# Kernel tuning notes

Hardware: AMD Instinct MI355X
Metric: run time of the kernel (lower is better)

## Reference

```python
import jax, jax.numpy as jnp
from jax import lax
import numpy as np

B, S, D_IN = 2048, 512, 5
H, E_DIM, N_EMB, C_CONV = 64, 32, 64, 32
COMMIT = 0.01


def _lstm_params(key, in_dim, hid):
    ks = jax.random.split(key, 4)
    sc = 1.0 / np.sqrt(hid)
    wih = jax.random.uniform(ks[0], (4 * hid, in_dim), minval=-sc, maxval=sc)
    whh = jax.random.uniform(ks[1], (4 * hid, hid), minval=-sc, maxval=sc)
    bih = jax.random.uniform(ks[2], (4 * hid,), minval=-sc, maxval=sc)
    bhh = jax.random.uniform(ks[3], (4 * hid,), minval=-sc, maxval=sc)
    return wih, whh, bih, bhh


def setup_inputs() -> dict:
    key = jax.random.key(0)
    ks = jax.random.split(key, 12)
    inp = {}
    inp['x'] = jax.random.normal(ks[0], (B, S, D_IN), dtype=jnp.float32)
    inp['conv_w'] = jax.random.normal(ks[1], (C_CONV, D_IN, 3)) * 0.2  # OIH
    inp['conv_b'] = jax.random.normal(ks[2], (C_CONV,)) * 0.05
    inp['bn_g'] = jnp.ones((C_CONV,)) + jax.random.normal(ks[3], (C_CONV,)) * 0.05
    inp['bn_b'] = jax.random.normal(ks[4], (C_CONV,)) * 0.05
    inp['bn_m'] = jax.random.normal(ks[5], (C_CONV,)) * 0.1
    inp['bn_v'] = jax.random.uniform(ks[6], (C_CONV,), minval=0.5, maxval=1.5)
    cw = _lstm_params(ks[7], C_CONV, H)
    cw1 = _lstm_params(jax.random.fold_in(ks[7], 1), H, H)
    vw = _lstm_params(ks[8], D_IN, H)
    vw1 = _lstm_params(jax.random.fold_in(ks[8], 1), H, H)
    for pre, p in (('cnn0', cw), ('cnn1', cw1), ('vq0', vw), ('vq1', vw1)):
        inp[pre + '_wih'], inp[pre + '_whh'], inp[pre + '_bih'], inp[pre + '_bhh'] = p
    inp['proj_w'] = jax.random.normal(ks[9], (E_DIM, H)) * (1.0 / np.sqrt(H))
    inp['proj_b'] = jax.random.normal(ks[10], (E_DIM,)) * 0.05
    xav = np.sqrt(6.0 / (N_EMB + E_DIM))
    inp['codebook'] = jax.random.uniform(ks[11], (N_EMB, E_DIM), minval=-xav, maxval=xav)
    return inp


def _lstm_layer(xs, wih, whh, bih, bhh):
    # xs: [S, B, in] -> (ys [S,B,H], h_final [B,H])
    b = xs.shape[1]
    h0 = jnp.zeros((b, H), xs.dtype)
    bias = bih + bhh

    def step(carry, x_t):
        h, c = carry
        gates = x_t @ wih.T + h @ whh.T + bias
        i, f, g, o = jnp.split(gates, 4, axis=-1)
        c = jax.nn.sigmoid(f) * c + jax.nn.sigmoid(i) * jnp.tanh(g)
        h = jax.nn.sigmoid(o) * jnp.tanh(c)
        return (h, c), h

    (h, c), ys = lax.scan(step, (h0, h0), xs)
    return ys, h


def _forward(x, conv_w, conv_b, bn_g, bn_b, bn_m, bn_v,
             cnn0_wih, cnn0_whh, cnn0_bih, cnn0_bhh,
             cnn1_wih, cnn1_whh, cnn1_bih, cnn1_bhh,
             vq0_wih, vq0_whh, vq0_bih, vq0_bhh,
             vq1_wih, vq1_whh, vq1_bih, vq1_bhh,
             proj_w, proj_b, codebook):
    # CNN stream: conv1d(k=3, pad=1) + BN (eval) + ReLU; dropout = identity (eval)
    x_ncw = jnp.transpose(x, (0, 2, 1))  # [B, D_IN, S]
    y = lax.conv_general_dilated(x_ncw, conv_w, (1,), [(1, 1)],
                                 dimension_numbers=('NCH', 'OIH', 'NCH'))
    y = y + conv_b[None, :, None]
    y = (y - bn_m[None, :, None]) * (bn_g / jnp.sqrt(bn_v + 1e-5))[None, :, None] + bn_b[None, :, None]
    y = jax.nn.relu(y)
    y = jnp.transpose(y, (2, 0, 1))  # [S, B, 32] time-major
    ys, _ = _lstm_layer(y, cnn0_wih, cnn0_whh, cnn0_bih, cnn0_bhh)
    _, cnn_features = _lstm_layer(ys, cnn1_wih, cnn1_whh, cnn1_bih, cnn1_bhh)  # [B, H]

    # VQ stream
    xt = jnp.transpose(x, (1, 0, 2))  # [S, B, D_IN]
    ys2, _ = _lstm_layer(xt, vq0_wih, vq0_whh, vq0_bih, vq0_bhh)
    _, vq_hidden = _lstm_layer(ys2, vq1_wih, vq1_whh, vq1_bih, vq1_bhh)  # [B, H]
    vq_proj = vq_hidden @ proj_w.T + proj_b  # [B, E_DIM]

    # Vector quantization
    d = (jnp.sum(vq_proj ** 2, axis=1, keepdims=True)
         + jnp.sum(codebook ** 2, axis=1)
         - 2.0 * vq_proj @ codebook.T)  # [B, N_EMB]
    idx = jnp.argmin(d, axis=1)
    quantized = codebook[idx]  # [B, E_DIM]
    e_loss = jnp.mean((lax.stop_gradient(quantized) - vq_proj) ** 2)
    q_loss = jnp.mean((quantized - lax.stop_gradient(vq_proj)) ** 2)
    vq_loss = q_loss + COMMIT * e_loss
    quantized = vq_proj + lax.stop_gradient(quantized - vq_proj)  # STE
    enc = jax.nn.one_hot(idx, N_EMB, dtype=vq_proj.dtype)
    avg_probs = jnp.mean(enc, axis=0)
    perplexity = jnp.exp(-jnp.sum(avg_probs * jnp.log(avg_probs + 1e-10)))

    combined = jnp.concatenate([cnn_features, quantized], axis=1)  # [B, H+E_DIM]
    return combined, vq_loss, perplexity


def reference(x, conv_w, conv_b, bn_g, bn_b, bn_m, bn_v,
              cnn0_wih, cnn0_whh, cnn0_bih, cnn0_bhh,
              cnn1_wih, cnn1_whh, cnn1_bih, cnn1_bhh,
              vq0_wih, vq0_whh, vq0_bih, vq0_bhh,
              vq1_wih, vq1_whh, vq1_bih, vq1_bhh,
              proj_w, proj_b, codebook):
    combined, vq_loss, perplexity = _forward(
        x, conv_w, conv_b, bn_g, bn_b, bn_m, bn_v,
        cnn0_wih, cnn0_whh, cnn0_bih, cnn0_bhh,
        cnn1_wih, cnn1_whh, cnn1_bih, cnn1_bhh,
        vq0_wih, vq0_whh, vq0_bih, vq0_bhh,
        vq1_wih, vq1_whh, vq1_bih, vq1_bhh,
        proj_w, proj_b, codebook)
    # num_classes=None -> returns (combined, combined, vq_loss, perplexity)
    return combined, combined, vq_loss, perplexity
```

## Files before the change

### kernel.cpp

```cpp
#include <hip/hip_runtime.h>
#include <math.h>
#include <stdint.h>

#define B_TOT 2048
#define SEQ   512
#define DIN   5
#define HID   64
#define EDIM  32
#define NEMB  64
#define BT    16
#define NBLK_STREAM 128
#define COMB  96
#define OUTC  (B_TOT*COMB)

typedef __attribute__((ext_vector_type(8))) _Float16 half8;
typedef __attribute__((ext_vector_type(4))) float float4v;

#if __has_builtin(__builtin_amdgcn_exp2f)
#define FEXP2(x) __builtin_amdgcn_exp2f(x)
#else
#define FEXP2(x) exp2f(x)
#endif
#if __has_builtin(__builtin_amdgcn_rcpf)
#define FRCP(x) __builtin_amdgcn_rcpf(x)
#else
#define FRCP(x) (1.0f/(x))
#endif

__device__ __forceinline__ float fsig(float x){
  return FRCP(1.0f + FEXP2(-1.44269504089f * x));
}
__device__ __forceinline__ float ftanh(float x){
  return fmaf(2.0f, FRCP(1.0f + FEXP2(-2.88539008178f * x)), -1.0f);
}
#define MFMA16(a,b,c) __builtin_amdgcn_mfma_f32_16x16x32_f16((a),(b),(c),0,0,0)

#define LOOP_BARRIER() do { \
    asm volatile("s_waitcnt lgkmcnt(0)" ::: "memory"); \
    __builtin_amdgcn_s_barrier(); \
  } while (0)

__global__ __launch_bounds__(256)
void conv_pre_kernel(const float* __restrict__ xg,
                     const float* __restrict__ conv_w, const float* __restrict__ conv_b,
                     const float* __restrict__ bn_g, const float* __restrict__ bn_b,
                     const float* __restrict__ bn_m, const float* __restrict__ bn_v,
                     _Float16* __restrict__ Y)
{
  __shared__ float wcs[16][32];
  const int tid = threadIdx.x;
  if (tid < 32) {
    float s = bn_g[tid] * rsqrtf(bn_v[tid] + 1e-5f);
#pragma unroll
    for (int i = 0; i < 5; ++i)
#pragma unroll
      for (int tau = 0; tau < 3; ++tau)
        wcs[tau*5 + i][tid] = conv_w[tid*15 + i*3 + tau] * s;
    wcs[15][tid] = (conv_b[tid] - bn_m[tid]) * s + bn_b[tid];
  }
  __syncthreads();
  const int total = B_TOT * SEQ;
  for (int idx = blockIdx.x*256 + tid; idx < total; idx += gridDim.x*256) {
    const int b = idx >> 9, t = idx & (SEQ-1);
    const float* xb = xg + ((size_t)b*SEQ + t)*DIN;
    float xm[5], x0[5], xp[5];
#pragma unroll
    for (int i = 0; i < 5; ++i) {
      x0[i] = xb[i];
      xm[i] = (t > 0)       ? xb[i - DIN] : 0.f;
      xp[i] = (t < SEQ-1)   ? xb[i + DIN] : 0.f;
    }
    _Float16 yv[32];
#pragma unroll
    for (int ch = 0; ch < 32; ++ch) {
      float s = wcs[15][ch];
#pragma unroll
      for (int i = 0; i < 5; ++i)
        s += wcs[i][ch]*xm[i] + wcs[5+i][ch]*x0[i] + wcs[10+i][ch]*xp[i];
      yv[ch] = (_Float16)fmaxf(s, 0.f);
    }
    half8* dst = (half8*)(Y + (size_t)idx*32);
#pragma unroll
    for (int g = 0; g < 4; ++g) dst[g] = *(half8*)&yv[g*8];
  }
}

template<bool PRE>
__global__ __launch_bounds__(1024)
__attribute__((amdgpu_waves_per_eu(4, 4)))
void fused_kernel(const float* __restrict__ xg,
                  const float* __restrict__ conv_w, const float* __restrict__ conv_b,
                  const float* __restrict__ bn_g, const float* __restrict__ bn_b,
                  const float* __restrict__ bn_m, const float* __restrict__ bn_v,
                  const float* __restrict__ cnn0_wih, const float* __restrict__ cnn0_whh,
                  const float* __restrict__ cnn0_bih, const float* __restrict__ cnn0_bhh,
                  const float* __restrict__ cnn1_wih, const float* __restrict__ cnn1_whh,
                  const float* __restrict__ cnn1_bih, const float* __restrict__ cnn1_bhh,
                  const float* __restrict__ vq0_wih, const float* __restrict__ vq0_whh,
                  const float* __restrict__ vq0_bih, const float* __restrict__ vq0_bhh,
                  const float* __restrict__ vq1_wih, const float* __restrict__ vq1_whh,
                  const float* __restrict__ vq1_bih, const float* __restrict__ vq1_bhh,
                  const float* __restrict__ proj_w, const float* __restrict__ proj_b,
                  const float* __restrict__ codebook, const _Float16* __restrict__ Yg,
                  float* __restrict__ out, float* __restrict__ ws_f,
                  int* __restrict__ ws_hist)
{
  __shared__ __align__(16) _Float16 ZT[2][5][4][BT][8];
  __shared__ __align__(16) float hfin[BT][HID];
  __shared__ __align__(16) float pbuf[BT][EDIM];
  __shared__ float xwin[4][BT][DIN];

  const int tid  = threadIdx.x;
  const bool is_cnn = (blockIdx.x < NBLK_STREAM);
  const int b0   = (is_cnn ? blockIdx.x : blockIdx.x - NBLK_STREAM) * BT;
  const int w    = tid >> 6;
  const int lane = tid & 63;
  const int n16  = lane & 15;
  const int quad = lane >> 4;
  const int u    = 4*w + quad;

  const float* wih0 = is_cnn ? cnn0_wih : vq0_wih;
  const float* whh0 = is_cnn ? cnn0_whh : vq0_whh;
  const float* bih0 = is_cnn ? cnn0_bih : vq0_bih;
  const float* bhh0 = is_cnn ? cnn0_bhh : vq0_bhh;
  const float* wih1 = is_cnn ? cnn1_wih : vq1_wih;
  const float* whh1 = is_cnn ? cnn1_whh : vq1_whh;
  const float* bih1 = is_cnn ? cnn1_bih : vq1_bih;
  const float* bhh1 = is_cnn ? cnn1_bhh : vq1_bhh;

  const int orow = 64*(n16 & 3) + 4*w + (n16 >> 2);
  half8 Ah0[3], Ah1[4];
#pragma unroll
  for (int kt = 0; kt < 3; ++kt) {
    half8 vh;
#pragma unroll
    for (int j = 0; j < 8; ++j) {
      const int g = kt*32 + quad*8 + j;
      float wv;
      if (is_cnn) wv = (g < 32) ? wih0[orow*32 + g] : whh0[orow*64 + (g-32)];
      else        wv = (g < 5) ? wih0[orow*5 + g] : (g < 32 ? 0.f : whh0[orow*64 + (g-32)]);
      vh[j] = (_Float16)wv;
    }
    Ah0[kt] = vh;
  }
#pragma unroll
  for (int kt = 0; kt < 4; ++kt) {
    half8 vh;
#pragma unroll
    for (int j = 0; j < 8; ++j) {
      const int g = kt*32 + quad*8 + j;
      float wv = (g < 64) ? wih1[orow*64 + g] : whh1[orow*64 + (g-64)];
      vh[j] = (_Float16)wv;
    }
    Ah1[kt] = vh;
  }

  float4v bc0, bc1;
#pragma unroll
  for (int r = 0; r < 4; ++r) {
    bc0[r] = bih0[64*r + u] + bhh0[64*r + u];
    bc1[r] = bih1[64*r + u] + bhh1[64*r + u];
  }

  float wr[16];
  if (!PRE) {
#pragma unroll
    for (int i = 0; i < 16; ++i) wr[i] = 0.f;
    if (is_cnn && tid < 512) {
      const int cc = tid >> 4;
      float s = bn_g[cc] * rsqrtf(bn_v[cc] + 1e-5f);
#pragma unroll
      for (int i = 0; i < 5; ++i)
#pragma unroll
        for (int tau = 0; tau < 3; ++tau)
          wr[tau*5 + i] = conv_w[cc*15 + i*3 + tau] * s;
      wr[15] = (conv_b[cc] - bn_m[cc]) * s + bn_b[cc];
    }
  }

  for (int i2 = tid; i2 < 2*5*4*BT*8/2; i2 += 1024) ((uint32_t*)ZT)[i2] = 0;

  const int xn = tid / 5, xi = tid % 5;
  const int yn = tid >> 2, ykg = tid & 3;
  float xpref = 0.f;
  half8 ypref{};
  const _Float16* Yb = nullptr;
  if (PRE && is_cnn && tid < 64)
    Yb = Yg + ((size_t)(b0 + yn)*SEQ)*32 + ykg*8;

  #define ZB(b) ((_Float16*)(&ZT[(b)][0][0][0][0]))
  #define ZIDX(tile,k32,n) (((tile)*4 + (((k32)>>3)&3))*(BT*8) + (n)*8 + ((k32)&7))

  if (!PRE && is_cnn) {
    if (tid < BT*DIN) {
#pragma unroll
      for (int j = 0; j < 4; ++j)
        xwin[j][xn][xi] = xg[((size_t)(b0+xn)*SEQ + j)*DIN + xi];
    }
  }
  __syncthreads();

  if (is_cnn) {
    if (PRE) {
      if (tid < 64) {
        half8 y0 = *(const half8*)(Yb + (size_t)0*32);
        half8 y1 = *(const half8*)(Yb + (size_t)1*32);
        ypref    = *(const half8*)(Yb + (size_t)2*32);
        *(half8*)&ZB(1)[ykg*(BT*8) + yn*8] = y0;
        *(half8*)&ZB(0)[ykg*(BT*8) + yn*8] = y1;
      }
    } else {
      if (tid < 512) {
        const int cc = tid >> 4, cn = tid & 15;
        float s = wr[15];
#pragma unroll
        for (int i = 0; i < 5; ++i)
          s += wr[5+i]*xwin[0][cn][i] + wr[10+i]*xwin[1][cn][i];
        s = fmaxf(s, 0.f);
        ZB(1)[ZIDX(0, cc, cn)] = (_Float16)s;
      }
    }
  } else {
    if (tid < BT*DIN) {
      float x0v = xg[((size_t)(b0+xn)*SEQ + 0)*DIN + xi];
      float x1v = xg[((size_t)(b0+xn)*SEQ + 1)*DIN + xi];
      ZB(1)[ZIDX(0, xi, xn)] = (_Float16)x0v;
      ZB(0)[ZIDX(0, xi, xn)] = (_Float16)x1v;
      xpref = xg[((size_t)(b0+xn)*SEQ + 2)*DIN + xi];
    }
  }
  __syncthreads();

  float c0 = 0.f, c1 = 0.f, h1v = 0.f;
  {
    half8 bt0 = *(const half8*)&ZT[1][0][quad][n16][0];
    half8 bt1 = *(const half8*)&ZT[1][1][quad][n16][0];
    half8 bt2 = *(const half8*)&ZT[1][2][quad][n16][0];
    float4v a0 = bc0;
    a0 = MFMA16(Ah0[0], bt0, a0);
    a0 = MFMA16(Ah0[1], bt1, a0);
    a0 = MFMA16(Ah0[2], bt2, a0);
    c0 = fsig(a0[1])*c0 + fsig(a0[0])*ftanh(a0[2]);
    float h0 = fsig(a0[3])*ftanh(c0);
    ZB(0)[ZIDX(1 + (u>>5), u & 31, n16)] = (_Float16)h0;
  }
  if (!PRE && is_cnn) {
    if (tid < 512) {
      const int cc = tid >> 4, cn = tid & 15;
      float s = wr[15];
#pragma unroll
      for (int i = 0; i < 5; ++i)
        s += wr[i]*xwin[0][cn][i] + wr[5+i]*xwin[1][cn][i]
           + wr[10+i]*xwin[2][cn][i];
      s = fmaxf(s, 0.f);
      ZB(0)[ZIDX(0, cc, cn)] = (_Float16)s;
    }
    if (tid < BT*DIN) xpref = xg[((size_t)(b0+xn)*SEQ + 4)*DIN + xi];
  }
  __syncthreads();

#pragma unroll 2
  for (int t = 0; t < SEQ; ++t) {
    const int rb = t & 1, wrb = rb ^ 1;
    half8 bt0 = *(const half8*)&ZT[rb][0][quad][n16][0];
    half8 bt1 = *(const half8*)&ZT[rb][1][quad][n16][0];
    half8 bt2 = *(const half8*)&ZT[rb][2][quad][n16][0];
    half8 bt3 = *(const half8*)&ZT[rb][3][quad][n16][0];
    half8 bt4 = *(const half8*)&ZT[rb][4][quad][n16][0];
    float4v a1 = bc1, a0 = bc0;
    a1 = MFMA16(Ah1[0], bt1, a1);
    a1 = MFMA16(Ah1[1], bt2, a1);
    a1 = MFMA16(Ah1[2], bt3, a1);
    a1 = MFMA16(Ah1[3], bt4, a1);
    a0 = MFMA16(Ah0[0], bt0, a0);
    a0 = MFMA16(Ah0[1], bt1, a0);
    a0 = MFMA16(Ah0[2], bt2, a0);

    {
      c1 = fsig(a1[1])*c1 + fsig(a1[0])*ftanh(a1[2]);
      float h1 = fsig(a1[3])*ftanh(c1);
      ZB(wrb)[ZIDX(3 + (u>>5), u & 31, n16)] = (_Float16)h1;
      if (is_cnn) h1v = h1;
      else if (t == SEQ-1) hfin[n16][u] = h1;
    }
    {
      c0 = fsig(a0[1])*c0 + fsig(a0[0])*ftanh(a0[2]);
      float h0 = fsig(a0[3])*ftanh(c0);
      ZB(wrb)[ZIDX(1 + (u>>5), u & 31, n16)] = (_Float16)h0;
    }
    if (is_cnn) {
      if (PRE) {
        if (tid < 64) {
          *(half8*)&ZB(wrb)[ykg*(BT*8) + yn*8] = ypref;
          const int tq = t + 3;
          if (tq < SEQ) ypref = *(const half8*)(Yb + (size_t)tq*32);
        }
      } else {
        if (tid < 512) {
          const int cc = tid >> 4, cn = tid & 15;
          const int s1 = (t+1)&3, s2 = (t+2)&3, s3 = (t+3)&3;
          float s = wr[15];
#pragma unroll
          for (int i = 0; i < 5; ++i)
            s += wr[i]*xwin[s1][cn][i] + wr[5+i]*xwin[s2][cn][i]
               + wr[10+i]*xwin[s3][cn][i];
          s = fmaxf(s, 0.f);
          ZB(wrb)[ZIDX(0, cc, cn)] = (_Float16)s;
        }
        if (tid < BT*DIN) {
          xwin[t & 3][xn][xi] = xpref;
          const int tq = t + 5;
          xpref = (tq < SEQ) ? xg[((size_t)(b0+xn)*SEQ + tq)*DIN + xi] : 0.f;
        }
      }
    } else {
      if (tid < BT*DIN) {
        ZB(wrb)[ZIDX(0, xi, xn)] = (_Float16)xpref;
        const int tq = t + 3;
        xpref = (tq < SEQ) ? xg[((size_t)(b0+xn)*SEQ + tq)*DIN + xi] : 0.f;
      }
    }
    LOOP_BARRIER();
  }

  if (is_cnn) {
    const size_t gb = (size_t)(b0 + n16);
    out[gb*COMB + u]        = h1v;
    out[OUTC + gb*COMB + u] = h1v;
  } else {
    if (tid < 512) {
      const int pn = tid >> 5, pe = tid & 31;
      float s = proj_b[pe];
      const float* pw = proj_w + pe*HID;
#pragma unroll
      for (int k = 0; k < HID; ++k) s += hfin[pn][k] * pw[k];
      pbuf[pn][pe] = s;
    }
    __syncthreads();
    {
      const int bb = w;
      const int nn = lane;
      const float* cbn = codebook + nn*EDIM;
      float d = 0.f;
#pragma unroll
      for (int k = 0; k < EDIM; ++k) { float df = pbuf[bb][k] - cbn[k]; d += df*df; }
      int bi = nn;
#pragma unroll
      for (int off = 32; off > 0; off >>= 1) {
        float od = __shfl_down(d, off, 64);
        int   oi = __shfl_down(bi, off, 64);
        if (od < d || (od == d && oi < bi)) { d = od; bi = oi; }
      }
      bi = __shfl(bi, 0, 64);
      float lv = 0.f;
      if (nn < EDIM) {
        float q = codebook[bi*EDIM + nn];
        const size_t gb = (size_t)(b0 + bb);
        out[gb*COMB + HID + nn]        = q;
        out[OUTC + gb*COMB + HID + nn] = q;
        float df = q - pbuf[bb][nn];
        lv = df*df;
      }
#pragma unroll
      for (int off = 32; off > 0; off >>= 1) lv += __shfl_down(lv, off, 64);
      if (nn == 0) { atomicAdd(ws_f, lv); atomicAdd(&ws_hist[bi], 1); }
    }
  }
}

__global__ void zero_ws_kernel(float* ws_f, int* ws_hist) {
  const int t = threadIdx.x;
  if (t == 0) ws_f[0] = 0.f;
  if (t < NEMB) ws_hist[t] = 0;
}

__global__ void vq_finalize_kernel(const float* __restrict__ ws_f,
                                   const int* __restrict__ ws_hist,
                                   float* __restrict__ out) {
  const int t = threadIdx.x;
  float p = (float)ws_hist[t] * (1.0f / (float)B_TOT);
  float e = -p * logf(p + 1e-10f);
#pragma unroll
  for (int off = 32; off > 0; off >>= 1) e += __shfl_down(e, off, 64);
  if (t == 0) {
    float mse = ws_f[0] * (1.0f / (float)(B_TOT * EDIM));
    out[2*OUTC + 0] = mse * 1.01f;
    out[2*OUTC + 1] = expf(e);
  }
}

extern "C" void kernel_launch(void* const* d_in, const int* in_sizes, int n_in,
                              void* d_out, int out_size, void* d_ws, size_t ws_size,
                              hipStream_t stream) {
  const float* x        = (const float*)d_in[0];
  const float* conv_w   = (const float*)d_in[1];
  const float* conv_b   = (const float*)d_in[2];
  const float* bn_g     = (const float*)d_in[3];
  const float* bn_b     = (const float*)d_in[4];
  const float* bn_m     = (const float*)d_in[5];
  const float* bn_v     = (const float*)d_in[6];
  const float* cnn0_wih = (const float*)d_in[7];
  const float* cnn0_whh = (const float*)d_in[8];
  const float* cnn0_bih = (const float*)d_in[9];
  const float* cnn0_bhh = (const float*)d_in[10];
  const float* cnn1_wih = (const float*)d_in[11];
  const float* cnn1_whh = (const float*)d_in[12];
  const float* cnn1_bih = (const float*)d_in[13];
  const float* cnn1_bhh = (const float*)d_in[14];
  const float* vq0_wih  = (const float*)d_in[15];
  const float* vq0_whh  = (const float*)d_in[16];
  const float* vq0_bih  = (const float*)d_in[17];
  const float* vq0_bhh  = (const float*)d_in[18];
  const float* vq1_wih  = (const float*)d_in[19];
  const float* vq1_whh  = (const float*)d_in[20];
  const float* vq1_bih  = (const float*)d_in[21];
  const float* vq1_bhh  = (const float*)d_in[22];
  const float* proj_w   = (const float*)d_in[23];
  const float* proj_b   = (const float*)d_in[24];
  const float* codebook = (const float*)d_in[25];

  float* out     = (float*)d_out;
  float* ws_f    = (float*)d_ws;
  int*   ws_hist = (int*)d_ws + 16;

  const size_t Y_BYTES = (size_t)B_TOT * SEQ * 32 * sizeof(_Float16);
  _Float16* Yg = (_Float16*)((char*)d_ws + 1024);
  const bool use_pre = (ws_size >= 1024 + Y_BYTES);

  hipLaunchKernelGGL(zero_ws_kernel, dim3(1), dim3(64), 0, stream, ws_f, ws_hist);
  if (use_pre) {
    hipLaunchKernelGGL(conv_pre_kernel, dim3(1024), dim3(256), 0, stream,
                       x, conv_w, conv_b, bn_g, bn_b, bn_m, bn_v, Yg);
    hipLaunchKernelGGL((fused_kernel<true>), dim3(2*NBLK_STREAM), dim3(1024), 0, stream,
                       x, conv_w, conv_b, bn_g, bn_b, bn_m, bn_v,
                       cnn0_wih, cnn0_whh, cnn0_bih, cnn0_bhh,
                       cnn1_wih, cnn1_whh, cnn1_bih, cnn1_bhh,
                       vq0_wih, vq0_whh, vq0_bih, vq0_bhh,
                       vq1_wih, vq1_whh, vq1_bih, vq1_bhh,
                       proj_w, proj_b, codebook, Yg, out, ws_f, ws_hist);
  } else {
    hipLaunchKernelGGL((fused_kernel<false>), dim3(2*NBLK_STREAM), dim3(1024), 0, stream,
                       x, conv_w, conv_b, bn_g, bn_b, bn_m, bn_v,
                       cnn0_wih, cnn0_whh, cnn0_bih, cnn0_bhh,
                       cnn1_wih, cnn1_whh, cnn1_bih, cnn1_bhh,
                       vq0_wih, vq0_whh, vq0_bih, vq0_bhh,
                       vq1_wih, vq1_whh, vq1_bih, vq1_bhh,
                       proj_w, proj_b, codebook, Yg, out, ws_f, ws_hist);
  }
  hipLaunchKernelGGL(vq_finalize_kernel, dim3(1), dim3(64), 0, stream, ws_f, ws_hist, out);
}
```

Before: 609.5 us.

## Fold bias into activations, split MFMA chains, fuse zero/finalize kernels, retile conv

```diff
diff --git a/kernel.cpp b/kernel.cpp
--- a/kernel.cpp
+++ b/kernel.cpp
@@ -14,6 +14,7 @@
 #define OUTC  (B_TOT*COMB)
 
 typedef __attribute__((ext_vector_type(8))) _Float16 half8;
+typedef __attribute__((ext_vector_type(4))) _Float16 half4;
 typedef __attribute__((ext_vector_type(4))) float float4v;
 
 #if __has_builtin(__builtin_amdgcn_exp2f)
@@ -27,11 +28,20 @@
 #define FRCP(x) (1.0f/(x))
 #endif
 
+#define L2E  1.44269504089f
+#define L2E2 2.88539008178f
+
+__device__ __forceinline__ float sig_b(float a, float bp){
+  return FRCP(1.0f + FEXP2(fmaf(a, -L2E, bp)));
+}
+__device__ __forceinline__ float tanh_b(float a, float bp){
+  return fmaf(2.0f, FRCP(1.0f + FEXP2(fmaf(a, -L2E2, bp))), -1.0f);
+}
+__device__ __forceinline__ float ftanh(float x){
+  return fmaf(2.0f, FRCP(1.0f + FEXP2(-L2E2 * x)), -1.0f);
+}
 __device__ __forceinline__ float fsig(float x){
-  return FRCP(1.0f + FEXP2(-1.44269504089f * x));
-}
-__device__ __forceinline__ float ftanh(float x){
-  return fmaf(2.0f, FRCP(1.0f + FEXP2(-2.88539008178f * x)), -1.0f);
+  return FRCP(1.0f + FEXP2(-L2E * x));
 }
 #define MFMA16(a,b,c) __builtin_amdgcn_mfma_f32_16x16x32_f16((a),(b),(c),0,0,0)
 
@@ -45,43 +55,52 @@
                      const float* __restrict__ conv_w, const float* __restrict__ conv_b,
                      const float* __restrict__ bn_g, const float* __restrict__ bn_b,
                      const float* __restrict__ bn_m, const float* __restrict__ bn_v,
-                     _Float16* __restrict__ Y)
+                     _Float16* __restrict__ Y,
+                     float* __restrict__ ws_f, int* __restrict__ ws_hist,
+                     int* __restrict__ ws_cnt)
 {
-  __shared__ float wcs[16][32];
   const int tid = threadIdx.x;
-  if (tid < 32) {
-    float s = bn_g[tid] * rsqrtf(bn_v[tid] + 1e-5f);
+  if (blockIdx.x == 0) {
+    if (tid == 0) ws_f[0] = 0.f;
+    if (tid < NEMB) ws_hist[tid] = 0;
+    if (tid == 64) ws_cnt[0] = 0;
+  }
+  const int cg = tid & 7;
+  const int it = tid >> 3;
+  float wv[4][15], bz[4];
+#pragma unroll
+  for (int j = 0; j < 4; ++j) {
+    const int ch = cg*4 + j;
+    const float s = bn_g[ch] * rsqrtf(bn_v[ch] + 1e-5f);
 #pragma unroll
     for (int i = 0; i < 5; ++i)
 #pragma unroll
       for (int tau = 0; tau < 3; ++tau)
-        wcs[tau*5 + i][tid] = conv_w[tid*15 + i*3 + tau] * s;
-    wcs[15][tid] = (conv_b[tid] - bn_m[tid]) * s + bn_b[tid];
-  }
-  __syncthreads();
-  const int total = B_TOT * SEQ;
-  for (int idx = blockIdx.x*256 + tid; idx < total; idx += gridDim.x*256) {
-    const int b = idx >> 9, t = idx & (SEQ-1);
-    const float* xb = xg + ((size_t)b*SEQ + t)*DIN;
+        wv[j][tau*5 + i] = conv_w[ch*15 + i*3 + tau] * s;
+    bz[j] = (conv_b[ch] - bn_m[ch]) * s + bn_b[ch];
+  }
+  const int ngrp = (B_TOT * SEQ) / 32;
+  for (int grp = blockIdx.x; grp < ngrp; grp += gridDim.x) {
+    const int idx = grp*32 + it;
+    const int t = idx & (SEQ-1);
+    const float* xb = xg + (size_t)idx*DIN;
     float xm[5], x0[5], xp[5];
 #pragma unroll
     for (int i = 0; i < 5; ++i) {
       x0[i] = xb[i];
-      xm[i] = (t > 0)       ? xb[i - DIN] : 0.f;
-      xp[i] = (t < SEQ-1)   ? xb[i + DIN] : 0.f;
-    }
-    _Float16 yv[32];
-#pragma unroll
-    for (int ch = 0; ch < 32; ++ch) {
-      float s = wcs[15][ch];
+      xm[i] = (t > 0)     ? xb[i - DIN] : 0.f;
+      xp[i] = (t < SEQ-1) ? xb[i + DIN] : 0.f;
+    }
+    half4 yv;
+#pragma unroll
+    for (int j = 0; j < 4; ++j) {
+      float s = bz[j];
 #pragma unroll
       for (int i = 0; i < 5; ++i)
-        s += wcs[i][ch]*xm[i] + wcs[5+i][ch]*x0[i] + wcs[10+i][ch]*xp[i];
-      yv[ch] = (_Float16)fmaxf(s, 0.f);
-    }
-    half8* dst = (half8*)(Y + (size_t)idx*32);
-#pragma unroll
-    for (int g = 0; g < 4; ++g) dst[g] = *(half8*)&yv[g*8];
+        s += wv[j][i]*xm[i] + wv[j][5+i]*x0[i] + wv[j][10+i]*xp[i];
+      yv[j] = (_Float16)fmaxf(s, 0.f);
+    }
+    *(half4*)(Y + (size_t)idx*32 + cg*4) = yv;
   }
 }
 
@@ -103,7 +122,7 @@
                   const float* __restrict__ proj_w, const float* __restrict__ proj_b,
                   const float* __restrict__ codebook, const _Float16* __restrict__ Yg,
                   float* __restrict__ out, float* __restrict__ ws_f,
-                  int* __restrict__ ws_hist)
+                  int* __restrict__ ws_hist, int* __restrict__ ws_cnt)
 {
   __shared__ __align__(16) _Float16 ZT[2][5][4][BT][8];
   __shared__ __align__(16) float hfin[BT][HID];
@@ -155,12 +174,14 @@
     Ah1[kt] = vh;
   }
 
-  float4v bc0, bc1;
+  float bp0[4], bp1[4];
 #pragma unroll
   for (int r = 0; r < 4; ++r) {
-    bc0[r] = bih0[64*r + u] + bhh0[64*r + u];
-    bc1[r] = bih1[64*r + u] + bhh1[64*r + u];
-  }
+    const float k = (r == 2) ? L2E2 : L2E;
+    bp0[r] = -k * (bih0[64*r + u] + bhh0[64*r + u]);
+    bp1[r] = -k * (bih1[64*r + u] + bhh1[64*r + u]);
+  }
+  const float4v zero4 = {0.f, 0.f, 0.f, 0.f};
 
   float wr[16];
   if (!PRE) {
@@ -236,12 +257,14 @@
     half8 bt0 = *(const half8*)&ZT[1][0][quad][n16][0];
     half8 bt1 = *(const half8*)&ZT[1][1][quad][n16][0];
     half8 bt2 = *(const half8*)&ZT[1][2][quad][n16][0];
-    float4v a0 = bc0;
-    a0 = MFMA16(Ah0[0], bt0, a0);
+    float4v a0 = MFMA16(Ah0[0], bt0, zero4);
     a0 = MFMA16(Ah0[1], bt1, a0);
     a0 = MFMA16(Ah0[2], bt2, a0);
-    c0 = fsig(a0[1])*c0 + fsig(a0[0])*ftanh(a0[2]);
-    float h0 = fsig(a0[3])*ftanh(c0);
+    float i0 = sig_b(a0[0], bp0[0]);
+    float g0 = tanh_b(a0[2], bp0[2]);
+    float o0 = sig_b(a0[3], bp0[3]);
+    c0 = i0 * g0;
+    float h0 = o0 * ftanh(c0);
     ZB(0)[ZIDX(1 + (u>>5), u & 31, n16)] = (_Float16)h0;
   }
   if (!PRE && is_cnn) {
@@ -267,25 +290,35 @@
     half8 bt2 = *(const half8*)&ZT[rb][2][quad][n16][0];
     half8 bt3 = *(const half8*)&ZT[rb][3][quad][n16][0];
     half8 bt4 = *(const half8*)&ZT[rb][4][quad][n16][0];
-    float4v a1 = bc1, a0 = bc0;
-    a1 = MFMA16(Ah1[0], bt1, a1);
-    a1 = MFMA16(Ah1[1], bt2, a1);
-    a1 = MFMA16(Ah1[2], bt3, a1);
-    a1 = MFMA16(Ah1[3], bt4, a1);
-    a0 = MFMA16(Ah0[0], bt0, a0);
-    a0 = MFMA16(Ah0[1], bt1, a0);
-    a0 = MFMA16(Ah0[2], bt2, a0);
-
+    float4v p1 = MFMA16(Ah1[0], bt1, zero4);
+    float4v q1 = MFMA16(Ah1[1], bt2, zero4);
+    float4v p0 = MFMA16(Ah0[0], bt0, zero4);
+    p1 = MFMA16(Ah1[2], bt3, p1);
+    q1 = MFMA16(Ah1[3], bt4, q1);
+    p0 = MFMA16(Ah0[1], bt1, p0);
+    p0 = MFMA16(Ah0[2], bt2, p0);
+
+    __builtin_amdgcn_s_setprio(1);
     {
-      c1 = fsig(a1[1])*c1 + fsig(a1[0])*ftanh(a1[2]);
-      float h1 = fsig(a1[3])*ftanh(c1);
+      float a1i = p1[0] + q1[0], a1f = p1[1] + q1[1];
+      float a1g = p1[2] + q1[2], a1o = p1[3] + q1[3];
+      float i1 = sig_b(a1i, bp1[0]);
+      float f1 = sig_b(a1f, bp1[1]);
+      float g1 = tanh_b(a1g, bp1[2]);
+      float o1 = sig_b(a1o, bp1[3]);
+      c1 = fmaf(f1, c1, i1 * g1);
+      float h1 = o1 * ftanh(c1);
       ZB(wrb)[ZIDX(3 + (u>>5), u & 31, n16)] = (_Float16)h1;
       if (is_cnn) h1v = h1;
       else if (t == SEQ-1) hfin[n16][u] = h1;
     }
     {
-      c0 = fsig(a0[1])*c0 + fsig(a0[0])*ftanh(a0[2]);
-      float h0 = fsig(a0[3])*ftanh(c0);
+      float i0 = sig_b(p0[0], bp0[0]);
+      float f0 = sig_b(p0[1], bp0[1]);
+      float g0 = tanh_b(p0[2], bp0[2]);
+      float o0 = sig_b(p0[3], bp0[3]);
+      c0 = fmaf(f0, c0, i0 * g0);
+      float h0 = o0 * ftanh(c0);
       ZB(wrb)[ZIDX(1 + (u>>5), u & 31, n16)] = (_Float16)h0;
     }
     if (is_cnn) {
@@ -320,6 +353,7 @@
         xpref = (tq < SEQ) ? xg[((size_t)(b0+xn)*SEQ + tq)*DIN + xi] : 0.f;
       }
     }
+    __builtin_amdgcn_s_setprio(0);
     LOOP_BARRIER();
   }
 
@@ -365,28 +399,34 @@
       for (int off = 32; off > 0; off >>= 1) lv += __shfl_down(lv, off, 64);
       if (nn == 0) { atomicAdd(ws_f, lv); atomicAdd(&ws_hist[bi], 1); }
     }
-  }
-}
-
-__global__ void zero_ws_kernel(float* ws_f, int* ws_hist) {
+    if (w == 0) {
+      __threadfence();
+      int c = 0;
+      if (lane == 0) c = atomicAdd(ws_cnt, 1);
+      c = __shfl(c, 0, 64);
+      if (c == NBLK_STREAM - 1) {
+        __threadfence();
+        int hv = atomicAdd(&ws_hist[lane], 0);
+        float p = (float)hv * (1.0f / (float)B_TOT);
+        float e = -p * logf(p + 1e-10f);
+#pragma unroll
+        for (int off = 32; off > 0; off >>= 1) e += __shfl_down(e, off, 64);
+        if (lane == 0) {
+          float wf = atomicAdd(ws_f, 0.0f);
+          float mse = wf * (1.0f / (float)(B_TOT * EDIM));
+          out[2*OUTC + 0] = mse * 1.01f;
+          out[2*OUTC + 1] = expf(e);
+        }
+      }
+    }
+  }
+}
+
+__global__ void zero_ws_kernel(float* ws_f, int* ws_hist, int* ws_cnt) {
   const int t = threadIdx.x;
   if (t == 0) ws_f[0] = 0.f;
   if (t < NEMB) ws_hist[t] = 0;
-}
-
-__global__ void vq_finalize_kernel(const float* __restrict__ ws_f,
-                                   const int* __restrict__ ws_hist,
-                                   float* __restrict__ out) {
-  const int t = threadIdx.x;
-  float p = (float)ws_hist[t] * (1.0f / (float)B_TOT);
-  float e = -p * logf(p + 1e-10f);
-#pragma unroll
-  for (int off = 32; off > 0; off >>= 1) e += __shfl_down(e, off, 64);
-  if (t == 0) {
-    float mse = ws_f[0] * (1.0f / (float)(B_TOT * EDIM));
-    out[2*OUTC + 0] = mse * 1.01f;
-    out[2*OUTC + 1] = expf(e);
-  }
+  if (t == 64) ws_cnt[0] = 0;
 }
 
 extern "C" void kernel_launch(void* const* d_in, const int* in_sizes, int n_in,
@@ -422,30 +462,31 @@
   float* out     = (float*)d_out;
   float* ws_f    = (float*)d_ws;
   int*   ws_hist = (int*)d_ws + 16;
+  int*   ws_cnt  = (int*)d_ws + 88;
 
   const size_t Y_BYTES = (size_t)B_TOT * SEQ * 32 * sizeof(_Float16);
   _Float16* Yg = (_Float16*)((char*)d_ws + 1024);
   const bool use_pre = (ws_size >= 1024 + Y_BYTES);
 
-  hipLaunchKernelGGL(zero_ws_kernel, dim3(1), dim3(64), 0, stream, ws_f, ws_hist);
   if (use_pre) {
-    hipLaunchKernelGGL(conv_pre_kernel, dim3(1024), dim3(256), 0, stream,
-                       x, conv_w, conv_b, bn_g, bn_b, bn_m, bn_v, Yg);
+    hipLaunchKernelGGL(conv_pre_kernel, dim3(2048), dim3(256), 0, stream,
+                       x, conv_w, conv_b, bn_g, bn_b, bn_m, bn_v, Yg,
+                       ws_f, ws_hist, ws_cnt);
     hipLaunchKernelGGL((fused_kernel<true>), dim3(2*NBLK_STREAM), dim3(1024), 0, stream,
                        x, conv_w, conv_b, bn_g, bn_b, bn_m, bn_v,
                        cnn0_wih, cnn0_whh, cnn0_bih, cnn0_bhh,
                        cnn1_wih, cnn1_whh, cnn1_bih, cnn1_bhh,
                        vq0_wih, vq0_whh, vq0_bih, vq0_bhh,
                        vq1_wih, vq1_whh, vq1_bih, vq1_bhh,
-                       proj_w, proj_b, codebook, Yg, out, ws_f, ws_hist);
+                       proj_w, proj_b, codebook, Yg, out, ws_f, ws_hist, ws_cnt);
   } else {
+    hipLaunchKernelGGL(zero_ws_kernel, dim3(1), dim3(128), 0, stream, ws_f, ws_hist, ws_cnt);
     hipLaunchKernelGGL((fused_kernel<false>), dim3(2*NBLK_STREAM), dim3(1024), 0, stream,
                        x, conv_w, conv_b, bn_g, bn_b, bn_m, bn_v,
                        cnn0_wih, cnn0_whh, cnn0_bih, cnn0_bhh,
                        cnn1_wih, cnn1_whh, cnn1_bih, cnn1_bhh,
                        vq0_wih, vq0_whh, vq0_bih, vq0_bhh,
                        vq1_wih, vq1_whh, vq1_bih, vq1_bhh,
-                       proj_w, proj_b, codebook, Yg, out, ws_f, ws_hist);
-  }
-  hipLaunchKernelGGL(vq_finalize_kernel, dim3(1), dim3(64), 0, stream, ws_f, ws_hist, out);
-}
+                       proj_w, proj_b, codebook, Yg, out, ws_f, ws_hist, ws_cnt);
+  }
+}
```

Result: faster. 570.1 us (-6.5%).
